# Kernel tuning notes

Hardware: AMD Instinct MI355X
Metric: run time of the kernel (lower is better)

Reference implementation:

```python
import jax, jax.numpy as jnp
import numpy as np


def _ragged_reverse(x, lengths):
    # x: [N, L, C]; flip the first `lengths[n]` steps of each sample, zero-fill the rest.
    N, L, C = x.shape
    t = jnp.arange(L, dtype=lengths.dtype)[None, :]          # [1, L]
    Ln = lengths[:, None]                                     # [N, 1]
    valid = t < Ln                                            # [N, L]
    idx = jnp.where(valid, Ln - 1 - t, 0)                     # [N, L]
    rev = jnp.take_along_axis(x, idx[:, :, None], axis=1)     # [N, L, C]
    return jnp.where(valid[:, :, None], rev, jnp.zeros((), x.dtype))


def _gru(xb, W_ih, W_hh, b_ih, b_hh):
    # xb: [B, L, C] -> outputs [B, L, H] (standard torch GRU cell math).
    B, L, C = xb.shape
    H = W_hh.shape[0]
    xw = xb @ W_ih + b_ih                                     # [B, L, 3H], input proj done once

    def step(h, xw_t):
        gh = h @ W_hh + b_hh                                  # [B, 3H]
        xr, xz, xn = jnp.split(xw_t, 3, axis=-1)
        hr, hz, hn = jnp.split(gh, 3, axis=-1)
        r = jax.nn.sigmoid(xr + hr)
        z = jax.nn.sigmoid(xz + hz)
        n = jnp.tanh(xn + r * hn)
        h_new = (1.0 - z) * n + z * h
        return h_new, h_new

    h0 = jnp.zeros((B, H), xb.dtype)
    _, ys = jax.lax.scan(step, h0, jnp.swapaxes(xw, 0, 1))    # ys: [L, B, H]
    return jnp.swapaxes(ys, 0, 1)                             # [B, L, H]


def reference(x, lengths, W_ih, W_hh, b_ih, b_hh):
    N, L, C = x.shape
    # to_bidirection: stack [forward; ragged-reversed] along batch -> [2N, L, C]
    rev = _ragged_reverse(x, lengths)
    xb = jnp.concatenate([x, rev], axis=0)
    out = _gru(xb, W_ih, W_hh, b_ih, b_hh)                    # [2N, L, H]
    # from_bidirection: split halves, concat on feature dim -> [N, L, 2H]
    return jnp.concatenate([out[:N], out[N:]], axis=2)


def setup_inputs() -> dict:
    key = jax.random.key(0)
    ks = jax.random.split(key, 6)
    N, L, C, H = 32, 2048, 64, 128
    s = 1.0 / np.sqrt(H)
    return {
        "x": jax.random.normal(ks[0], (N, L, C), dtype=jnp.float32),
        "lengths": jax.random.randint(ks[1], (N,), 1, L + 1, dtype=jnp.int32),
        "W_ih": jax.random.normal(ks[2], (C, 3 * H), dtype=jnp.float32) * s,
        "W_hh": jax.random.normal(ks[3], (H, 3 * H), dtype=jnp.float32) * s,
        "b_ih": jax.random.normal(ks[4], (3 * H,), dtype=jnp.float32) * s,
        "b_hh": jax.random.normal(ks[5], (3 * H,), dtype=jnp.float32) * s,
    }
```

## Files before the change

### kernel.cpp

```cpp
#include <hip/hip_runtime.h>

#define L_SEQ 2048
#define C_IN  64
#define HH    128
#define NSEQ  32
#define B2    64
#define G3    384
#define RING  16
#define XW32  (C_IN / 2)
#define XTOT  (NSEQ * L_SEQ * XW32)

typedef _Float16 half2_t __attribute__((ext_vector_type(2)));

#define PINU(v) asm volatile("" : "+v"(v))
#define STEP_BARRIER() asm volatile("s_waitcnt lgkmcnt(0)\n\ts_barrier" ::: "memory")

__device__ __forceinline__ float fdot2u(unsigned int a, unsigned int b, float c) {
    return __builtin_amdgcn_fdot2(__builtin_bit_cast(half2_t, a),
                                  __builtin_bit_cast(half2_t, b), c, false);
}

__device__ __forceinline__ unsigned int pack_h2(float a, float b) {
    half2_t t; t.x = (_Float16)a; t.y = (_Float16)b;
    return __builtin_bit_cast(unsigned int, t);
}

__device__ __forceinline__ float qadd1(float x) {
    int t = __builtin_amdgcn_update_dpp(0, __builtin_bit_cast(int, x),
                                        0xB1, 0xF, 0xF, true);
    return x + __builtin_bit_cast(float, t);
}

__device__ __forceinline__ float fast_sigmoid(float x) {
    float e = __builtin_amdgcn_exp2f(-1.4426950408889634f * x);
    return __builtin_amdgcn_rcpf(1.0f + e);
}

__device__ __forceinline__ float fast_tanh(float x) {
    float a = fabsf(x);
    float e = __builtin_amdgcn_exp2f(-2.8853900817779268f * a);
    float r = (1.0f - e) * __builtin_amdgcn_rcpf(1.0f + e);
    return copysignf(r, x);
}

__device__ __forceinline__ float pdot32(const unsigned int (&w)[32],
                                        const unsigned int* __restrict__ xrow,
                                        float acc) {
    const uint4* x4 = (const uint4*)xrow;
#pragma unroll
    for (int i = 0; i < 8; ++i) {
        const uint4 v = x4[i];
        acc = fdot2u(v.x, w[4*i+0], acc);
        acc = fdot2u(v.y, w[4*i+1], acc);
        acc = fdot2u(v.z, w[4*i+2], acc);
        acc = fdot2u(v.w, w[4*i+3], acc);
    }
    return acc;
}

__global__ __launch_bounds__(256)
void pack_x_kernel(const float* __restrict__ x, unsigned int* __restrict__ xh)
{
    const size_t i = (size_t)blockIdx.x * 256 + threadIdx.x;
    if (i < (size_t)XTOT) {
        const float2 v = ((const float2*)x)[i];
        xh[i] = pack_h2(v.x, v.y);
    }
    if (i < XW32) xh[(size_t)XTOT + i] = 0u;
}

__global__ __launch_bounds__(512) __attribute__((amdgpu_waves_per_eu(1, 1)))
void bigru_fused(const unsigned int* __restrict__ xh,
                 const int* __restrict__ lengths,
                 const float* __restrict__ W_ih, const float* __restrict__ W_hh,
                 const float* __restrict__ b_ih, const float* __restrict__ b_hh,
                 float* __restrict__ out)
{
    __shared__ unsigned int hbufu[2][64];
    __shared__ float        ring[RING][G3];

    const int tid = threadIdx.x;
    const int s   = blockIdx.x;
    const bool isFwd = (s < NSEQ);
    const int  len   = isFwd ? L_SEQ : lengths[s - NSEQ];
    const unsigned int* __restrict__ xseq = xh + (size_t)(s % NSEQ) * L_SEQ * XW32;
    const unsigned int* __restrict__ zrow = xh + (size_t)XTOT;

    const bool consumer = (tid < 256);
    const int u = tid & 255;
    const int j = u >> 1;
    const int p = u & 1;

    unsigned int w0[32], w1[32], w2[32];
    float bA = 0.f, bB = 0.f;

    if (consumer) {
        const float* Wb = W_hh + (size_t)(64 * p) * G3;
#pragma unroll
        for (int k = 0; k < 32; ++k) {
            w0[k] = pack_h2(Wb[(2*k) * G3 + j],       Wb[(2*k+1) * G3 + j]);
            w1[k] = pack_h2(Wb[(2*k) * G3 + 128 + j], Wb[(2*k+1) * G3 + 128 + j]);
            w2[k] = pack_h2(Wb[(2*k) * G3 + 256 + j], Wb[(2*k+1) * G3 + 256 + j]);
        }
#pragma unroll
        for (int k = 0; k < 32; ++k) { PINU(w0[k]); PINU(w1[k]); PINU(w2[k]); }
        bA = b_hh[256 + j];
        if (tid < 64) hbufu[0][tid] = 0u;
    } else {
#pragma unroll
        for (int k = 0; k < 32; ++k)
            w0[k] = pack_h2(W_ih[(2*k) * G3 + u], W_ih[(2*k+1) * G3 + u]);
        bA = b_ih[u] + b_hh[u];
        if (u >= 128) {
            const int c1 = 128 + u;
#pragma unroll
            for (int k = 0; k < 32; ++k)
                w1[k] = pack_h2(W_ih[(2*k) * G3 + c1], W_ih[(2*k+1) * G3 + c1]);
            bB = b_ih[c1];
        }
#pragma unroll
        for (int k = 0; k < 32; ++k) { PINU(w0[k]); PINU(w1[k]); }

        for (int rd = 0; rd < 6; ++rd) {
            const int srcL = isFwd ? rd : (len - 1 - rd);
            const unsigned int* xrow =
                (srcL >= 0) ? (xseq + (size_t)srcL * XW32) : zrow;
            ring[rd][u] = pdot32(w0, xrow, bA);
            if (u >= 128) ring[rd][128 + u] = pdot32(w1, xrow, bB);
        }
    }
    __syncthreads();

    float cr = 0.f, cz = 0.f, cn = 0.f, hreg = 0.f;
    if (consumer) { cr = ring[0][j]; cz = ring[0][128 + j]; cn = ring[0][256 + j]; }

    float* outbase = out + (size_t)(s % NSEQ) * L_SEQ * 256 + (isFwd ? 0 : HH);
    int cur = 0;

    for (int t = 0; t < L_SEQ; ++t) {
        if (consumer) {
            const int sln = (t + 1) & (RING - 1);
            const float nr = ring[sln][j];
            const float nz = ring[sln][128 + j];
            const float nn = ring[sln][256 + j];
            float ar = 0.f, az = 0.f, an = 0.f;
            const uint4* hb = (const uint4*)&hbufu[cur][p * 32];
#pragma unroll
            for (int i = 0; i < 8; ++i) {
                const uint4 hv = hb[i];
                ar = fdot2u(hv.x, w0[4*i+0], ar); ar = fdot2u(hv.y, w0[4*i+1], ar);
                ar = fdot2u(hv.z, w0[4*i+2], ar); ar = fdot2u(hv.w, w0[4*i+3], ar);
                az = fdot2u(hv.x, w1[4*i+0], az); az = fdot2u(hv.y, w1[4*i+1], az);
                az = fdot2u(hv.z, w1[4*i+2], az); az = fdot2u(hv.w, w1[4*i+3], az);
                an = fdot2u(hv.x, w2[4*i+0], an); an = fdot2u(hv.y, w2[4*i+1], an);
                an = fdot2u(hv.z, w2[4*i+2], an); an = fdot2u(hv.w, w2[4*i+3], an);
            }
            ar = qadd1(ar); az = qadd1(az); an = qadd1(an);
            const float r = fast_sigmoid(cr + ar);
            const float z = fast_sigmoid(cz + az);
            const float n = fast_tanh(cn + r * (an + bA));
            const float hnew = z * (hreg - n) + n;
            hreg = hnew;
            if (p == 0) {
                ((_Float16*)&hbufu[cur ^ 1][0])[j] = (_Float16)hnew;
                outbase[(size_t)t * 256 + j] = hnew;
            }
            cur ^= 1;
            cr = nr; cz = nz; cn = nn;
        } else {
            const int rd = t + 6;
            if (rd < L_SEQ) {
                const int srcL = isFwd ? rd : (len - 1 - rd);
                const unsigned int* xrow =
                    (srcL >= 0) ? (xseq + (size_t)srcL * XW32) : zrow;
                const int sl = rd & (RING - 1);
                ring[sl][u] = pdot32(w0, xrow, bA);
                if (u >= 128) ring[sl][128 + u] = pdot32(w1, xrow, bB);
            }
        }
        STEP_BARRIER();
    }
}

extern "C" void kernel_launch(void* const* d_in, const int* in_sizes, int n_in,
                              void* d_out, int out_size, void* d_ws, size_t ws_size,
                              hipStream_t stream) {
    const float* x       = (const float*)d_in[0];
    const int*   lengths = (const int*)  d_in[1];
    const float* W_ih    = (const float*)d_in[2];
    const float* W_hh    = (const float*)d_in[3];
    const float* b_ih    = (const float*)d_in[4];
    const float* b_hh    = (const float*)d_in[5];
    float* out = (float*)d_out;

    unsigned int* xh = (unsigned int*)d_ws;

    pack_x_kernel<<<dim3((XTOT + 255) / 256), dim3(256), 0, stream>>>(x, xh);
    bigru_fused<<<dim3(B2), dim3(512), 0, stream>>>(
        xh, lengths, W_ih, W_hh, b_ih, b_hh, out);
}
```

Before: 1.149 ms.

## Compute input projection with MFMA in batches of 16 steps inside recurrent warps

Removes the separate producer warps and has the 256 recurrent threads compute the input projection themselves, 16 timesteps at a time, using 16x16x32 f16 MFMA into a 48-slot LDS ring. Global loads for the next batch are issued ahead, and the hidden-state dot product is split into two independent accumulator chains to shorten the dependency chain. The goal is to halve the block size and cut per-step barrier cost. The price is periodic bursts of MFMA work on the critical recurrent path every 16 steps, plus more register pressure from holding the MFMA weight fragments.

```diff
diff --git a/kernel.cpp b/kernel.cpp
--- a/kernel.cpp
+++ b/kernel.cpp
@@ -6,56 +6,41 @@
 #define NSEQ  32
 #define B2    64
 #define G3    384
-#define RING  16
 #define XW32  (C_IN / 2)
 #define XTOT  (NSEQ * L_SEQ * XW32)
-
+#define RSLOT 48
+#define RG    130
+
+typedef _Float16 f16x8 __attribute__((ext_vector_type(8)));
+typedef float    f32x4 __attribute__((ext_vector_type(4)));
 typedef _Float16 half2_t __attribute__((ext_vector_type(2)));
 
 #define PINU(v) asm volatile("" : "+v"(v))
 #define STEP_BARRIER() asm volatile("s_waitcnt lgkmcnt(0)\n\ts_barrier" ::: "memory")
+#define MFMA16(a, b, c) __builtin_amdgcn_mfma_f32_16x16x32_f16((a), (b), (c), 0, 0, 0)
 
 __device__ __forceinline__ float fdot2u(unsigned int a, unsigned int b, float c) {
     return __builtin_amdgcn_fdot2(__builtin_bit_cast(half2_t, a),
                                   __builtin_bit_cast(half2_t, b), c, false);
 }
-
 __device__ __forceinline__ unsigned int pack_h2(float a, float b) {
     half2_t t; t.x = (_Float16)a; t.y = (_Float16)b;
     return __builtin_bit_cast(unsigned int, t);
 }
-
 __device__ __forceinline__ float qadd1(float x) {
     int t = __builtin_amdgcn_update_dpp(0, __builtin_bit_cast(int, x),
                                         0xB1, 0xF, 0xF, true);
     return x + __builtin_bit_cast(float, t);
 }
-
 __device__ __forceinline__ float fast_sigmoid(float x) {
     float e = __builtin_amdgcn_exp2f(-1.4426950408889634f * x);
     return __builtin_amdgcn_rcpf(1.0f + e);
 }
-
 __device__ __forceinline__ float fast_tanh(float x) {
     float a = fabsf(x);
     float e = __builtin_amdgcn_exp2f(-2.8853900817779268f * a);
     float r = (1.0f - e) * __builtin_amdgcn_rcpf(1.0f + e);
     return copysignf(r, x);
-}
-
-__device__ __forceinline__ float pdot32(const unsigned int (&w)[32],
-                                        const unsigned int* __restrict__ xrow,
-                                        float acc) {
-    const uint4* x4 = (const uint4*)xrow;
-#pragma unroll
-    for (int i = 0; i < 8; ++i) {
-        const uint4 v = x4[i];
-        acc = fdot2u(v.x, w[4*i+0], acc);
-        acc = fdot2u(v.y, w[4*i+1], acc);
-        acc = fdot2u(v.z, w[4*i+2], acc);
-        acc = fdot2u(v.w, w[4*i+3], acc);
-    }
-    return acc;
 }
 
 __global__ __launch_bounds__(256)
@@ -69,7 +54,7 @@
     if (i < XW32) xh[(size_t)XTOT + i] = 0u;
 }
 
-__global__ __launch_bounds__(512) __attribute__((amdgpu_waves_per_eu(1, 1)))
+__global__ __launch_bounds__(256) __attribute__((amdgpu_waves_per_eu(1, 1)))
 void bigru_fused(const unsigned int* __restrict__ xh,
                  const int* __restrict__ lengths,
                  const float* __restrict__ W_ih, const float* __restrict__ W_hh,
@@ -77,108 +62,147 @@
                  float* __restrict__ out)
 {
     __shared__ unsigned int hbufu[2][64];
-    __shared__ float        ring[RING][G3];
+    __shared__ float ring[RSLOT][3][RG];
 
     const int tid = threadIdx.x;
     const int s   = blockIdx.x;
-    const bool isFwd = (s < NSEQ);
-    const int  len   = isFwd ? L_SEQ : lengths[s - NSEQ];
-    const unsigned int* __restrict__ xseq = xh + (size_t)(s % NSEQ) * L_SEQ * XW32;
-    const unsigned int* __restrict__ zrow = xh + (size_t)XTOT;
-
-    const bool consumer = (tid < 256);
-    const int u = tid & 255;
-    const int j = u >> 1;
-    const int p = u & 1;
-
-    unsigned int w0[32], w1[32], w2[32];
-    float bA = 0.f, bB = 0.f;
-
-    if (consumer) {
+    const bool fwd = (s < NSEQ);
+    const int  len = fwd ? L_SEQ : lengths[s - NSEQ];
+    const unsigned int* __restrict__ xbase = xh + (size_t)(s % NSEQ) * L_SEQ * XW32;
+    const unsigned int* __restrict__ zrow  = xh + (size_t)XTOT;
+
+    const int j = tid >> 1;
+    const int p = tid & 1;
+    const int w  = tid >> 6;
+    const int l  = tid & 63;
+    const int lm = l & 15;
+    const int lg = l >> 4;
+
+    unsigned int wr[32], wz[32], wn[32];
+    {
         const float* Wb = W_hh + (size_t)(64 * p) * G3;
 #pragma unroll
         for (int k = 0; k < 32; ++k) {
-            w0[k] = pack_h2(Wb[(2*k) * G3 + j],       Wb[(2*k+1) * G3 + j]);
-            w1[k] = pack_h2(Wb[(2*k) * G3 + 128 + j], Wb[(2*k+1) * G3 + 128 + j]);
-            w2[k] = pack_h2(Wb[(2*k) * G3 + 256 + j], Wb[(2*k+1) * G3 + 256 + j]);
-        }
-#pragma unroll
-        for (int k = 0; k < 32; ++k) { PINU(w0[k]); PINU(w1[k]); PINU(w2[k]); }
-        bA = b_hh[256 + j];
-        if (tid < 64) hbufu[0][tid] = 0u;
-    } else {
-#pragma unroll
-        for (int k = 0; k < 32; ++k)
-            w0[k] = pack_h2(W_ih[(2*k) * G3 + u], W_ih[(2*k+1) * G3 + u]);
-        bA = b_ih[u] + b_hh[u];
-        if (u >= 128) {
-            const int c1 = 128 + u;
-#pragma unroll
-            for (int k = 0; k < 32; ++k)
-                w1[k] = pack_h2(W_ih[(2*k) * G3 + c1], W_ih[(2*k+1) * G3 + c1]);
-            bB = b_ih[c1];
-        }
-#pragma unroll
-        for (int k = 0; k < 32; ++k) { PINU(w0[k]); PINU(w1[k]); }
-
-        for (int rd = 0; rd < 6; ++rd) {
-            const int srcL = isFwd ? rd : (len - 1 - rd);
-            const unsigned int* xrow =
-                (srcL >= 0) ? (xseq + (size_t)srcL * XW32) : zrow;
-            ring[rd][u] = pdot32(w0, xrow, bA);
-            if (u >= 128) ring[rd][128 + u] = pdot32(w1, xrow, bB);
-        }
+            wr[k] = pack_h2(Wb[(2*k) * G3 + j],       Wb[(2*k+1) * G3 + j]);
+            wz[k] = pack_h2(Wb[(2*k) * G3 + 128 + j], Wb[(2*k+1) * G3 + 128 + j]);
+            wn[k] = pack_h2(Wb[(2*k) * G3 + 256 + j], Wb[(2*k+1) * G3 + 256 + j]);
+        }
+#pragma unroll
+        for (int k = 0; k < 32; ++k) { PINU(wr[k]); PINU(wz[k]); PINU(wn[k]); }
     }
+    float bn = b_hh[256 + j];
+    PINU(bn);
+
+    f16x8 Bx[3][2][2];
+    float pbias[3][2];
+#pragma unroll
+    for (int g = 0; g < 3; ++g)
+#pragma unroll
+        for (int e = 0; e < 2; ++e) {
+            const int gc = g * 128 + 32 * w + 16 * e + lm;
+            pbias[g][e] = b_ih[gc] + ((g < 2) ? b_hh[gc] : 0.f);
+#pragma unroll
+            for (int kt = 0; kt < 2; ++kt) {
+                f16x8 f;
+#pragma unroll
+                for (int i = 0; i < 8; ++i)
+                    f[i] = (_Float16)W_ih[(kt * 32 + lg * 8 + i) * G3 + gc];
+                Bx[g][e][kt] = f;
+            }
+        }
+
+    uint4 AxP0, AxP1;
+    auto loadA = [&](int rowBase) {
+        const int row = rowBase + lm;
+        const int src = fwd ? row : (len - 1 - row);
+        const unsigned int* ptr = ((unsigned)src < (unsigned)L_SEQ)
+                                ? (xbase + (size_t)src * XW32) : zrow;
+        AxP0 = *(const uint4*)(ptr + lg * 4);
+        AxP1 = *(const uint4*)(ptr + 16 + lg * 4);
+    };
+    auto produce = [&](int s0) {
+        const f16x8 A0 = __builtin_bit_cast(f16x8, AxP0);
+        const f16x8 A1 = __builtin_bit_cast(f16x8, AxP1);
+#pragma unroll
+        for (int g = 0; g < 3; ++g)
+#pragma unroll
+            for (int e = 0; e < 2; ++e) {
+                f32x4 acc = {pbias[g][e], pbias[g][e], pbias[g][e], pbias[g][e]};
+                acc = MFMA16(A0, Bx[g][e][0], acc);
+                acc = MFMA16(A1, Bx[g][e][1], acc);
+                const int colw = 32 * w + 16 * e + lm;
+#pragma unroll
+                for (int q = 0; q < 4; ++q)
+                    ring[s0 + lg * 4 + q][g][colw] = acc[q];
+            }
+    };
+
+    float hreg = 0.f;
+    if (tid < 64) hbufu[0][tid] = 0u;
+
+    loadA(0);  produce(0);
+    loadA(16); produce(16);
+    loadA(32);
     __syncthreads();
 
-    float cr = 0.f, cz = 0.f, cn = 0.f, hreg = 0.f;
-    if (consumer) { cr = ring[0][j]; cz = ring[0][128 + j]; cn = ring[0][256 + j]; }
-
-    float* outbase = out + (size_t)(s % NSEQ) * L_SEQ * 256 + (isFwd ? 0 : HH);
+    float cr = ring[0][0][j], cz = ring[0][1][j], cn = ring[0][2][j];
+
+    float* outbase = out + (size_t)(s % NSEQ) * L_SEQ * 256 + (fwd ? 0 : HH);
     int cur = 0;
+    int slotN = 1;
+    int s0 = 32;
 
     for (int t = 0; t < L_SEQ; ++t) {
-        if (consumer) {
-            const int sln = (t + 1) & (RING - 1);
-            const float nr = ring[sln][j];
-            const float nz = ring[sln][128 + j];
-            const float nn = ring[sln][256 + j];
-            float ar = 0.f, az = 0.f, an = 0.f;
-            const uint4* hb = (const uint4*)&hbufu[cur][p * 32];
-#pragma unroll
-            for (int i = 0; i < 8; ++i) {
-                const uint4 hv = hb[i];
-                ar = fdot2u(hv.x, w0[4*i+0], ar); ar = fdot2u(hv.y, w0[4*i+1], ar);
-                ar = fdot2u(hv.z, w0[4*i+2], ar); ar = fdot2u(hv.w, w0[4*i+3], ar);
-                az = fdot2u(hv.x, w1[4*i+0], az); az = fdot2u(hv.y, w1[4*i+1], az);
-                az = fdot2u(hv.z, w1[4*i+2], az); az = fdot2u(hv.w, w1[4*i+3], az);
-                an = fdot2u(hv.x, w2[4*i+0], an); an = fdot2u(hv.y, w2[4*i+1], an);
-                an = fdot2u(hv.z, w2[4*i+2], an); an = fdot2u(hv.w, w2[4*i+3], an);
-            }
-            ar = qadd1(ar); az = qadd1(az); an = qadd1(an);
-            const float r = fast_sigmoid(cr + ar);
-            const float z = fast_sigmoid(cz + az);
-            const float n = fast_tanh(cn + r * (an + bA));
-            const float hnew = z * (hreg - n) + n;
-            hreg = hnew;
-            if (p == 0) {
-                ((_Float16*)&hbufu[cur ^ 1][0])[j] = (_Float16)hnew;
-                outbase[(size_t)t * 256 + j] = hnew;
-            }
-            cur ^= 1;
-            cr = nr; cz = nz; cn = nn;
-        } else {
-            const int rd = t + 6;
-            if (rd < L_SEQ) {
-                const int srcL = isFwd ? rd : (len - 1 - rd);
-                const unsigned int* xrow =
-                    (srcL >= 0) ? (xseq + (size_t)srcL * XW32) : zrow;
-                const int sl = rd & (RING - 1);
-                ring[sl][u] = pdot32(w0, xrow, bA);
-                if (u >= 128) ring[sl][128 + u] = pdot32(w1, xrow, bB);
-            }
+        if ((t & 15) == 8) {
+            if (t + 24 < L_SEQ) produce(s0);
+            s0 += 16; if (s0 >= RSLOT) s0 -= RSLOT;
+            if (t + 40 < L_SEQ) loadA(t + 40);
+        }
+
+        const float nr = ring[slotN][0][j];
+        const float nz = ring[slotN][1][j];
+        const float nn = ring[slotN][2][j];
+        ++slotN; if (slotN == RSLOT) slotN = 0;
+
+        float arA = 0.f, azA = 0.f, anA = 0.f;
+        float arB = 0.f, azB = 0.f, anB = 0.f;
+        const uint4* hb = (const uint4*)&hbufu[cur][p * 32];
+#pragma unroll
+        for (int i = 0; i < 4; ++i) {
+            const uint4 hv = hb[i];
+            arA = fdot2u(hv.x, wr[4*i+0], arA); arA = fdot2u(hv.y, wr[4*i+1], arA);
+            arA = fdot2u(hv.z, wr[4*i+2], arA); arA = fdot2u(hv.w, wr[4*i+3], arA);
+            azA = fdot2u(hv.x, wz[4*i+0], azA); azA = fdot2u(hv.y, wz[4*i+1], azA);
+            azA = fdot2u(hv.z, wz[4*i+2], azA); azA = fdot2u(hv.w, wz[4*i+3], azA);
+            anA = fdot2u(hv.x, wn[4*i+0], anA); anA = fdot2u(hv.y, wn[4*i+1], anA);
+            anA = fdot2u(hv.z, wn[4*i+2], anA); anA = fdot2u(hv.w, wn[4*i+3], anA);
+        }
+#pragma unroll
+        for (int i = 4; i < 8; ++i) {
+            const uint4 hv = hb[i];
+            arB = fdot2u(hv.x, wr[4*i+0], arB); arB = fdot2u(hv.y, wr[4*i+1], arB);
+            arB = fdot2u(hv.z, wr[4*i+2], arB); arB = fdot2u(hv.w, wr[4*i+3], arB);
+            azB = fdot2u(hv.x, wz[4*i+0], azB); azB = fdot2u(hv.y, wz[4*i+1], azB);
+            azB = fdot2u(hv.z, wz[4*i+2], azB); azB = fdot2u(hv.w, wz[4*i+3], azB);
+            anB = fdot2u(hv.x, wn[4*i+0], anB); anB = fdot2u(hv.y, wn[4*i+1], anB);
+            anB = fdot2u(hv.z, wn[4*i+2], anB); anB = fdot2u(hv.w, wn[4*i+3], anB);
+        }
+        float ar = arA + arB, az = azA + azB, an = anA + anB;
+        ar = qadd1(ar); az = qadd1(az); an = qadd1(an);
+
+        const float r = fast_sigmoid(cr + ar);
+        const float z = fast_sigmoid(cz + az);
+        const float n = fast_tanh(cn + r * (an + bn));
+        const float hnew = z * (hreg - n) + n;
+        hreg = hnew;
+
+        if (p == 0) {
+            ((_Float16*)&hbufu[cur ^ 1][0])[j] = (_Float16)hnew;
+            outbase[(size_t)t * 256 + j] = hnew;
         }
         STEP_BARRIER();
+        cur ^= 1;
+        cr = nr; cz = nz; cn = nn;
     }
 }
 
@@ -196,6 +220,6 @@
     unsigned int* xh = (unsigned int*)d_ws;
 
     pack_x_kernel<<<dim3((XTOT + 255) / 256), dim3(256), 0, stream>>>(x, xh);
-    bigru_fused<<<dim3(B2), dim3(512), 0, stream>>>(
+    bigru_fused<<<dim3(B2), dim3(256), 0, stream>>>(
         xh, lengths, W_ih, W_hh, b_ih, b_hh, out);
 }
```

After: 945.3 us (median of 2 runs). 1.22x faster.
